# Kernel tuning notes

Hardware: AMD Instinct MI355X
Metric: run time of the kernel (lower is better)

## Reference

```python
import jax, jax.numpy as jnp
import numpy as np

NUM_VIEWS = 24
SLOPE = 0.2
P = 14 * 14  # 196 spatial features per view
OUT = 1024


def setup_inputs() -> dict:
    key = jax.random.key(0)
    ks = jax.random.split(key, 6)
    B = 16384
    x = jax.random.normal(ks[0], (B, 14, 14, NUM_VIEWS), dtype=jnp.float32)
    indices = jax.random.randint(ks[1], (NUM_VIEWS,), 0, NUM_VIEWS, dtype=jnp.int64)
    # fc_idx: Linear(num_views -> 196); fc_aggre: Linear(392 -> 1024)
    W_idx = jax.random.normal(ks[2], (P, NUM_VIEWS), dtype=jnp.float32) * (1.0 / np.sqrt(NUM_VIEWS))
    b_idx = jax.random.normal(ks[3], (P,), dtype=jnp.float32) * 0.01
    W_aggre = jax.random.normal(ks[4], (OUT, 2 * P), dtype=jnp.float32) * (1.0 / np.sqrt(2 * P))
    b_aggre = jax.random.normal(ks[5], (OUT,), dtype=jnp.float32) * 0.01
    return {"x": x, "indices": indices, "W_idx": W_idx, "b_idx": b_idx,
            "W_aggre": W_aggre, "b_aggre": b_aggre}


def reference(x, indices, W_idx, b_idx, W_aggre, b_aggre):
    B, s1, s2, s3 = x.shape
    K = indices.shape[0]
    xr = x.reshape(B, s1 * s2, s3)            # [B, 196, V]
    # one-hot index path is batch-independent: compute once per idx
    oh = jax.nn.one_hot(indices, s3, dtype=x.dtype)                # [K, V]
    infer_index = jax.nn.leaky_relu(oh @ W_idx.T + b_idx, SLOPE)   # [K, 196]
    x_sel = jnp.take(xr, indices, axis=2)                          # [B, 196, K]
    # fc_aggre(cat(x_part, idx_part)) summed over K, split weight by halves
    Wx = W_aggre[:, :s1 * s2]   # [1024, 196] acts on x part
    Wi = W_aggre[:, s1 * s2:]   # [1024, 196] acts on index part
    out_x = jnp.einsum('bpk,op->bo', x_sel, Wx)                    # [B, 1024]
    out_i = infer_index.sum(axis=0) @ Wi.T                         # [1024]
    out = out_x + out_i + K * b_aggre                              # broadcast over batch
    return out
```

## Files before the change

### kernel.cpp

```cpp
#include <hip/hip_runtime.h>

#define B_ROWS 16384
#define PDIM 196
#define KPAD 224
#define NV 24
#define OUT_DIM 1024
#define SLOPE 0.2f

#define RED_BLOCKS (B_ROWS * KPAD / 256)

typedef __attribute__((ext_vector_type(8))) short short8;
typedef __attribute__((ext_vector_type(4))) float floatx4;

static __device__ __forceinline__ unsigned short f2bf(float f) {
    union { float f; unsigned int u; } v; v.f = f;
    unsigned int r = v.u + 0x7fffu + ((v.u >> 16) & 1u);
    return (unsigned short)(r >> 16);
}

__global__ __launch_bounds__(256) void reduce_prep(
        const float* __restrict__ x,
        const int* __restrict__ idx,
        const float* __restrict__ W_idx,
        const float* __restrict__ b_idx,
        const float* __restrict__ W_aggre,
        const float* __restrict__ b_aggre,
        unsigned short* __restrict__ Sm,
        unsigned short* __restrict__ Bp,
        float* __restrict__ cvec) {
    int t = threadIdx.x;
    if (blockIdx.x < RED_BLOCKS) {
        __shared__ float scnt[NV];
        if (t < NV) {
            int c = 0;
            #pragma unroll
            for (int k = 0; k < NV; ++k) c += (idx[k] == t);
            scnt[t] = (float)c;
        }
        __syncthreads();
        unsigned g = blockIdx.x * 256u + t;
        unsigned row = g / KPAD;
        unsigned p = g - row * KPAD;
        float a = 0.f;
        if (p < PDIM) {
            const float4* x4 = (const float4*)(x + ((size_t)row * PDIM + p) * NV);
            #pragma unroll
            for (int i = 0; i < 6; ++i) {
                float4 q = x4[i];
                a += scnt[4 * i + 0] * q.x + scnt[4 * i + 1] * q.y +
                     scnt[4 * i + 2] * q.z + scnt[4 * i + 3] * q.w;
            }
        }
        unsigned rt = row >> 4, l15 = row & 15;
        unsigned ks = p >> 5, quad = (p >> 3) & 3, j = p & 7;
        size_t addr = (((size_t)rt * 7 + ks) * 64 + quad * 16 + l15) * 8 + j;
        Sm[addr] = (p < PDIM) ? f2bf(a) : (unsigned short)0;
    } else if (blockIdx.x < RED_BLOCKS + 112) {
        int tid = (blockIdx.x - RED_BLOCKS) * 256 + t;
        int ks = tid >> 12;
        int rem = tid & 4095;
        int nt = rem >> 6;
        int lane = rem & 63;
        int n = nt * 16 + (lane & 15);
        int kb = ks * 32 + (lane >> 4) * 8;
        unsigned short* dst = Bp + (size_t)tid * 8;
        #pragma unroll
        for (int j = 0; j < 8; ++j) {
            int k = kb + j;
            float v = (k < PDIM) ? W_aggre[(size_t)n * (2 * PDIM) + k] : 0.f;
            dst[j] = f2bf(v);
        }
    } else {
        __shared__ float v_sh[PDIM];
        __shared__ int idx_sh[NV];
        if (t < NV) idx_sh[t] = idx[t];
        __syncthreads();
        if (t < PDIM) {
            float bp = b_idx[t];
            float a = 0.f;
            #pragma unroll
            for (int k = 0; k < NV; ++k) {
                float z = W_idx[t * NV + idx_sh[k]] + bp;
                a += (z > 0.f) ? z : SLOPE * z;
            }
            v_sh[t] = a;
        }
        __syncthreads();
        int bc = blockIdx.x - (RED_BLOCKS + 112);
        int o = bc * 32 + (t >> 3);
        int pl = t & 7;
        const float* wr = W_aggre + (size_t)o * (2 * PDIM) + PDIM;
        float a = 0.f;
        for (int p = pl; p < PDIM; p += 8) a += v_sh[p] * wr[p];
        a += __shfl_down(a, 4, 8);
        a += __shfl_down(a, 2, 8);
        a += __shfl_down(a, 1, 8);
        if (pl == 0) cvec[o] = a + (float)NV * b_aggre[o];
    }
}

__global__ __launch_bounds__(256) void gemm_k(const unsigned short* __restrict__ Sm,
                                              const unsigned short* __restrict__ Bp,
                                              const float* __restrict__ cvec,
                                              float* __restrict__ out) {
    int tid = threadIdx.x;
    int lane = tid & 63, wave = tid >> 6;
    int wm = wave >> 1, wn = wave & 1;
    int quad = lane >> 4, l15 = lane & 15;
    int bm = blockIdx.y, bn = blockIdx.x;

    floatx4 acc[4][4];
    #pragma unroll
    for (int i = 0; i < 4; ++i)
        #pragma unroll
        for (int j = 0; j < 4; ++j)
            acc[i][j] = (floatx4){0.f, 0.f, 0.f, 0.f};

    int rt0 = bm * 8 + wm * 4;
    int ntg0 = bn * 8 + wn * 4;

    #pragma unroll
    for (int ks = 0; ks < 7; ++ks) {
        short8 af[4], bfr[4];
        #pragma unroll
        for (int mt = 0; mt < 4; ++mt) {
            const unsigned short* ap =
                Sm + (((size_t)(rt0 + mt) * 7 + ks) * 64 + lane) * 8;
            af[mt] = *(const short8*)ap;
        }
        #pragma unroll
        for (int nt = 0; nt < 4; ++nt) {
            const unsigned short* bp =
                Bp + ((size_t)((ks * 64 + ntg0 + nt) * 64 + lane)) * 8;
            bfr[nt] = *(const short8*)bp;
        }
        #pragma unroll
        for (int mt = 0; mt < 4; ++mt)
            #pragma unroll
            for (int nt = 0; nt < 4; ++nt)
                acc[mt][nt] = __builtin_amdgcn_mfma_f32_16x16x32_bf16(
                    af[mt], bfr[nt], acc[mt][nt], 0, 0, 0);
    }

    int colb = bn * 128 + wn * 64 + l15;
    #pragma unroll
    for (int nt = 0; nt < 4; ++nt) {
        float cv = cvec[colb + nt * 16];
        #pragma unroll
        for (int mt = 0; mt < 4; ++mt) {
            int row0 = (rt0 + mt) * 16 + quad * 4;
            float* po = out + (size_t)row0 * OUT_DIM + colb + nt * 16;
            po[0 * OUT_DIM] = acc[mt][nt][0] + cv;
            po[1 * OUT_DIM] = acc[mt][nt][1] + cv;
            po[2 * OUT_DIM] = acc[mt][nt][2] + cv;
            po[3 * OUT_DIM] = acc[mt][nt][3] + cv;
        }
    }
}

extern "C" void kernel_launch(void* const* d_in, const int* in_sizes, int n_in,
                              void* d_out, int out_size, void* d_ws, size_t ws_size,
                              hipStream_t stream) {
    const float* x       = (const float*)d_in[0];
    const int*   idx     = (const int*)d_in[1];
    const float* W_idx   = (const float*)d_in[2];
    const float* b_idx   = (const float*)d_in[3];
    const float* W_aggre = (const float*)d_in[4];
    const float* b_aggre = (const float*)d_in[5];
    float* out = (float*)d_out;

    char* ws = (char*)d_ws;
    float*          cvec = (float*)ws;
    unsigned short* Bp   = (unsigned short*)(ws + 4096);
    unsigned short* Sm   = (unsigned short*)(ws + 524288);

    hipLaunchKernelGGL(reduce_prep, dim3(RED_BLOCKS + 144), dim3(256), 0, stream,
                       x, idx, W_idx, b_idx, W_aggre, b_aggre, Sm, Bp, cvec);
    hipLaunchKernelGGL(gemm_k, dim3(8, 128), dim3(256), 0, stream,
                       Sm, Bp, cvec, out);
}
```

Before: 460.4 us.

## Fuse view-reduction into GEMM via shared-memory A tile per 16-row block

Moves the per-row weighted view reduction out of the prep kernel into the GEMM kernel. Each block now reduces 16 batch rows into a bf16 A tile in LDS, then every wave computes 256 output columns using MFMA with B fragments read from global memory. This removes the round trip of the intermediate Sm matrix through global memory, at the cost of small 16-row tiles. Each block also rereads the whole packed weight matrix from cache, and the reduction phase has little parallelism per block.

```diff
diff --git a/kernel.cpp b/kernel.cpp
--- a/kernel.cpp
+++ b/kernel.cpp
@@ -6,8 +6,6 @@
 #define NV 24
 #define OUT_DIM 1024
 #define SLOPE 0.2f
-
-#define RED_BLOCKS (B_ROWS * KPAD / 256)
 
 typedef __attribute__((ext_vector_type(8))) short short8;
 typedef __attribute__((ext_vector_type(4))) float floatx4;
@@ -18,45 +16,17 @@
     return (unsigned short)(r >> 16);
 }
 
-__global__ __launch_bounds__(256) void reduce_prep(
-        const float* __restrict__ x,
+__global__ __launch_bounds__(256) void prep_k(
         const int* __restrict__ idx,
         const float* __restrict__ W_idx,
         const float* __restrict__ b_idx,
         const float* __restrict__ W_aggre,
         const float* __restrict__ b_aggre,
-        unsigned short* __restrict__ Sm,
         unsigned short* __restrict__ Bp,
         float* __restrict__ cvec) {
     int t = threadIdx.x;
-    if (blockIdx.x < RED_BLOCKS) {
-        __shared__ float scnt[NV];
-        if (t < NV) {
-            int c = 0;
-            #pragma unroll
-            for (int k = 0; k < NV; ++k) c += (idx[k] == t);
-            scnt[t] = (float)c;
-        }
-        __syncthreads();
-        unsigned g = blockIdx.x * 256u + t;
-        unsigned row = g / KPAD;
-        unsigned p = g - row * KPAD;
-        float a = 0.f;
-        if (p < PDIM) {
-            const float4* x4 = (const float4*)(x + ((size_t)row * PDIM + p) * NV);
-            #pragma unroll
-            for (int i = 0; i < 6; ++i) {
-                float4 q = x4[i];
-                a += scnt[4 * i + 0] * q.x + scnt[4 * i + 1] * q.y +
-                     scnt[4 * i + 2] * q.z + scnt[4 * i + 3] * q.w;
-            }
-        }
-        unsigned rt = row >> 4, l15 = row & 15;
-        unsigned ks = p >> 5, quad = (p >> 3) & 3, j = p & 7;
-        size_t addr = (((size_t)rt * 7 + ks) * 64 + quad * 16 + l15) * 8 + j;
-        Sm[addr] = (p < PDIM) ? f2bf(a) : (unsigned short)0;
-    } else if (blockIdx.x < RED_BLOCKS + 112) {
-        int tid = (blockIdx.x - RED_BLOCKS) * 256 + t;
+    if (blockIdx.x < 112) {
+        int tid = blockIdx.x * 256 + t;
         int ks = tid >> 12;
         int rem = tid & 4095;
         int nt = rem >> 6;
@@ -86,7 +56,7 @@
             v_sh[t] = a;
         }
         __syncthreads();
-        int bc = blockIdx.x - (RED_BLOCKS + 112);
+        int bc = blockIdx.x - 112;
         int o = bc * 32 + (t >> 3);
         int pl = t & 7;
         const float* wr = W_aggre + (size_t)o * (2 * PDIM) + PDIM;
@@ -99,62 +69,77 @@
     }
 }
 
-__global__ __launch_bounds__(256) void gemm_k(const unsigned short* __restrict__ Sm,
-                                              const unsigned short* __restrict__ Bp,
-                                              const float* __restrict__ cvec,
-                                              float* __restrict__ out) {
-    int tid = threadIdx.x;
-    int lane = tid & 63, wave = tid >> 6;
-    int wm = wave >> 1, wn = wave & 1;
+__global__ __launch_bounds__(256) void fused_k(
+        const float* __restrict__ x,
+        const int* __restrict__ idx,
+        const unsigned short* __restrict__ Bp,
+        const float* __restrict__ cvec,
+        float* __restrict__ out) {
+    __shared__ float scnt[NV];
+    __shared__ unsigned short sA[7 * 64 * 8] __attribute__((aligned(16)));
+    int t = threadIdx.x;
+    int bg = blockIdx.x;
+
+    if (t < NV) {
+        int c = 0;
+        #pragma unroll
+        for (int k = 0; k < NV; ++k) c += (idx[k] == t);
+        scnt[t] = (float)c;
+    }
+    __syncthreads();
+
+    #pragma unroll 4
+    for (int i = 0; i < 14; ++i) {
+        int sl = t + 256 * i;
+        unsigned row16 = (unsigned)sl / 224u;
+        unsigned p = (unsigned)sl - row16 * 224u;
+        float a = 0.f;
+        if (p < PDIM) {
+            const float4* x4 = (const float4*)(x + ((size_t)(bg * 16 + row16) * PDIM + p) * NV);
+            #pragma unroll
+            for (int q = 0; q < 6; ++q) {
+                float4 v = x4[q];
+                a += scnt[4 * q + 0] * v.x + scnt[4 * q + 1] * v.y +
+                     scnt[4 * q + 2] * v.z + scnt[4 * q + 3] * v.w;
+            }
+        }
+        unsigned ks = p >> 5, qd = (p >> 3) & 3, j = p & 7;
+        sA[(ks * 64 + qd * 16 + row16) * 8 + j] = (p < PDIM) ? f2bf(a) : (unsigned short)0;
+    }
+    __syncthreads();
+
+    int lane = t & 63, wave = t >> 6;
     int quad = lane >> 4, l15 = lane & 15;
-    int bm = blockIdx.y, bn = blockIdx.x;
 
-    floatx4 acc[4][4];
+    short8 af[7];
     #pragma unroll
-    for (int i = 0; i < 4; ++i)
-        #pragma unroll
-        for (int j = 0; j < 4; ++j)
-            acc[i][j] = (floatx4){0.f, 0.f, 0.f, 0.f};
+    for (int ks = 0; ks < 7; ++ks)
+        af[ks] = *(const short8*)(sA + (ks * 64 + lane) * 8);
 
-    int rt0 = bm * 8 + wm * 4;
-    int ntg0 = bn * 8 + wn * 4;
+    floatx4 acc[16];
+    #pragma unroll
+    for (int nt = 0; nt < 16; ++nt) acc[nt] = (floatx4){0.f, 0.f, 0.f, 0.f};
 
+    const unsigned short* bbase = Bp + ((size_t)(wave * 16) * 64 + lane) * 8;
     #pragma unroll
     for (int ks = 0; ks < 7; ++ks) {
-        short8 af[4], bfr[4];
         #pragma unroll
-        for (int mt = 0; mt < 4; ++mt) {
-            const unsigned short* ap =
-                Sm + (((size_t)(rt0 + mt) * 7 + ks) * 64 + lane) * 8;
-            af[mt] = *(const short8*)ap;
+        for (int nt = 0; nt < 16; ++nt) {
+            short8 bf = *(const short8*)(bbase + (size_t)(ks * 64 + nt) * 64 * 8);
+            acc[nt] = __builtin_amdgcn_mfma_f32_16x16x32_bf16(af[ks], bf, acc[nt], 0, 0, 0);
         }
-        #pragma unroll
-        for (int nt = 0; nt < 4; ++nt) {
-            const unsigned short* bp =
-                Bp + ((size_t)((ks * 64 + ntg0 + nt) * 64 + lane)) * 8;
-            bfr[nt] = *(const short8*)bp;
-        }
-        #pragma unroll
-        for (int mt = 0; mt < 4; ++mt)
-            #pragma unroll
-            for (int nt = 0; nt < 4; ++nt)
-                acc[mt][nt] = __builtin_amdgcn_mfma_f32_16x16x32_bf16(
-                    af[mt], bfr[nt], acc[mt][nt], 0, 0, 0);
     }
 
-    int colb = bn * 128 + wn * 64 + l15;
+    int row0 = bg * 16 + quad * 4;
+    float* orow = out + (size_t)row0 * OUT_DIM + wave * 256 + l15;
     #pragma unroll
-    for (int nt = 0; nt < 4; ++nt) {
-        float cv = cvec[colb + nt * 16];
-        #pragma unroll
-        for (int mt = 0; mt < 4; ++mt) {
-            int row0 = (rt0 + mt) * 16 + quad * 4;
-            float* po = out + (size_t)row0 * OUT_DIM + colb + nt * 16;
-            po[0 * OUT_DIM] = acc[mt][nt][0] + cv;
-            po[1 * OUT_DIM] = acc[mt][nt][1] + cv;
-            po[2 * OUT_DIM] = acc[mt][nt][2] + cv;
-            po[3 * OUT_DIM] = acc[mt][nt][3] + cv;
-        }
+    for (int nt = 0; nt < 16; ++nt) {
+        float cv = cvec[wave * 256 + nt * 16 + l15];
+        float* po = orow + nt * 16;
+        po[0 * OUT_DIM] = acc[nt][0] + cv;
+        po[1 * OUT_DIM] = acc[nt][1] + cv;
+        po[2 * OUT_DIM] = acc[nt][2] + cv;
+        po[3 * OUT_DIM] = acc[nt][3] + cv;
     }
 }
 
@@ -172,10 +157,9 @@
     char* ws = (char*)d_ws;
     float*          cvec = (float*)ws;
     unsigned short* Bp   = (unsigned short*)(ws + 4096);
-    unsigned short* Sm   = (unsigned short*)(ws + 524288);
 
-    hipLaunchKernelGGL(reduce_prep, dim3(RED_BLOCKS + 144), dim3(256), 0, stream,
-                       x, idx, W_idx, b_idx, W_aggre, b_aggre, Sm, Bp, cvec);
-    hipLaunchKernelGGL(gemm_k, dim3(8, 128), dim3(256), 0, stream,
-                       Sm, Bp, cvec, out);
+    hipLaunchKernelGGL(prep_k, dim3(144), dim3(256), 0, stream,
+                       idx, W_idx, b_idx, W_aggre, b_aggre, Bp, cvec);
+    hipLaunchKernelGGL(fused_k, dim3(B_ROWS / 16), dim3(256), 0, stream,
+                       x, idx, Bp, cvec, out);
 }
```

After: 497.0 us. +7.9%, slower.
